# Optimization experiments

Hardware: AMD Instinct MI355X
Metric: run time of the kernel (lower is better)

The kernel has to match this reference:

```python
import jax, jax.numpy as jnp
import numpy as np
import math

T, C = 8192, 1024

def setup_inputs() -> dict:
    key = jax.random.key(0)
    ks = jax.random.split(key, 10)
    s = 1.0 / math.sqrt(C)
    return {
        "x": jax.random.normal(ks[0], (T, C), dtype=jnp.float32),
        "Wq": jax.random.normal(ks[1], (C, C), dtype=jnp.float32) * s,
        "bq": jax.random.normal(ks[2], (C,), dtype=jnp.float32) * s,
        "Wk": jax.random.normal(ks[3], (C, C), dtype=jnp.float32) * s,
        "bk": jax.random.normal(ks[4], (C,), dtype=jnp.float32) * s,
        "Wv": jax.random.normal(ks[5], (C, C), dtype=jnp.float32) * s,
        "bv": jax.random.normal(ks[6], (C,), dtype=jnp.float32) * s,
        "Wp": jax.random.normal(ks[7], (C, C), dtype=jnp.float32) * s,
        "bp": jax.random.normal(ks[8], (C,), dtype=jnp.float32) * s,
    }

def reference(x, Wq, bq, Wk, bk, Wv, bv, Wp, bp):
    # Single-head causal self-attention over an unbatched (T, C) sequence.
    t, c = x.shape
    q = x @ Wq.T + bq          # (T, C)
    k = x @ Wk.T + bk          # (T, C)
    v = x @ Wv.T + bv          # (T, C)
    att = (q @ k.T) / math.sqrt(c)                      # (T, T)
    causal = jnp.tril(jnp.ones((t, t), dtype=bool))
    att = jnp.where(causal, att, -jnp.inf)
    att = jax.nn.softmax(att, axis=-1)
    y = att @ v                                         # (T, C)
    y = y @ Wp.T + bp
    return y
```

## Files before the change

kernel.cpp:

```cpp
#include <hip/hip_runtime.h>
#include <hip/hip_bf16.h>

typedef __bf16 bf16x8 __attribute__((ext_vector_type(8)));
typedef float f32x4 __attribute__((ext_vector_type(4)));

static constexpr int Tn = 8192;
static constexpr int Cn = 1024;

#define DEVI __device__ __forceinline__

DEVI float bf2f(ushort u) { union { uint i; float f; } c; c.i = ((uint)u) << 16; return c.f; }
DEVI ushort f2bf(float f) {
  uint x = __builtin_bit_cast(uint, f);
  x += 0x7fffu + ((x >> 16) & 1u);
  return (ushort)(x >> 16);
}

typedef const __attribute__((address_space(1))) void glb_v;
typedef __attribute__((address_space(3))) void lds_v;

__global__ __launch_bounds__(256) void cast_all(
    const float* __restrict__ x, const float* __restrict__ wq, const float* __restrict__ wk,
    const float* __restrict__ wv, const float* __restrict__ wp,
    ushort* __restrict__ xb, ushort* __restrict__ wqb, ushort* __restrict__ wkb,
    ushort* __restrict__ wvb, ushort* __restrict__ wpb)
{
  const long long NX = (long long)Tn * Cn;
  const long long NW = (long long)Cn * Cn;
  long long i = ((long long)blockIdx.x * 256 + threadIdx.x) * 4;
  const float* src; ushort* dst; long long off;
  if (i < NX) { src = x; dst = xb; off = i; }
  else {
    long long r = i - NX; int seg = (int)(r >> 20); off = r & (NW - 1);
    src = seg == 0 ? wq : seg == 1 ? wk : seg == 2 ? wv : wp;
    dst = seg == 0 ? wqb : seg == 1 ? wkb : seg == 2 ? wvb : wpb;
  }
  float4 v = *reinterpret_cast<const float4*>(src + off);
  ushort4 o; o.x = f2bf(v.x); o.y = f2bf(v.y); o.z = f2bf(v.z); o.w = f2bf(v.w);
  *reinterpret_cast<ushort4*>(dst + off) = o;
}

template<bool OUT_BF16, bool HAS_BIAS, bool CAUSAL_SKIP, bool KLIMIT>
__global__ __launch_bounds__(256, 2)
void gemm_bt(const ushort* __restrict__ A, const ushort* __restrict__ Bt,
             const float* __restrict__ bias, void* __restrict__ outp,
             int M, int N, int K, float scale)
{
  const int bx = blockIdx.x;
  int by = KLIMIT ? (gridDim.y - 1 - blockIdx.y) : blockIdx.y;
  if (CAUSAL_SKIP && by < bx) return;

  __shared__ ushort Als[128 * 64];
  __shared__ ushort Bls[128 * 64];

  const int tid = threadIdx.x;
  const int lane = tid & 63;
  const int wid = tid >> 6;
  const int wr = (wid >> 1) * 64, wc = (wid & 1) * 64;
  const int ln15 = lane & 15, lhi = lane >> 4;
  const int aRow0 = by * 128, bCol0 = bx * 128;

  int Keff = K;
  if (KLIMIT) { int lim = (by + 1) * 128; Keff = lim < K ? lim : K; }
  const int nkt = Keff >> 6;

  f32x4 acc[4][4] = {};

  for (int kt = 0; kt < nkt; ++kt) {
    const int k0 = kt << 6;
#pragma unroll
    for (int i = 0; i < 4; ++i) {
      int c = tid + i * 256;
      int row = c >> 3, kc = c & 7;
      int kcs = kc ^ (row & 7);
      const ushort* ga = A + (size_t)(aRow0 + row) * (size_t)K + (k0 + kcs * 8);
      const ushort* gb = Bt + (size_t)(bCol0 + row) * (size_t)K + (k0 + kcs * 8);
      __builtin_amdgcn_global_load_lds((glb_v*)ga, (lds_v*)(&Als[c * 8]), 16, 0, 0);
      __builtin_amdgcn_global_load_lds((glb_v*)gb, (lds_v*)(&Bls[c * 8]), 16, 0, 0);
    }
    __syncthreads();
#pragma unroll
    for (int kk = 0; kk < 2; ++kk) {
      bf16x8 af[4], bfr[4];
#pragma unroll
      for (int mi = 0; mi < 4; ++mi) {
        int r = wr + mi * 16 + ln15;
        int kc = kk * 4 + lhi;
        int slot = r * 8 + (kc ^ (r & 7));
        af[mi] = *reinterpret_cast<const bf16x8*>(&Als[slot * 8]);
      }
#pragma unroll
      for (int ni = 0; ni < 4; ++ni) {
        int r = wc + ni * 16 + ln15;
        int kc = kk * 4 + lhi;
        int slot = r * 8 + (kc ^ (r & 7));
        bfr[ni] = *reinterpret_cast<const bf16x8*>(&Bls[slot * 8]);
      }
#pragma unroll
      for (int mi = 0; mi < 4; ++mi)
#pragma unroll
        for (int ni = 0; ni < 4; ++ni)
          acc[mi][ni] = __builtin_amdgcn_mfma_f32_16x16x32_bf16(af[mi], bfr[ni], acc[mi][ni], 0, 0, 0);
    }
    __syncthreads();
  }

#pragma unroll
  for (int ni = 0; ni < 4; ++ni) {
    int col = bCol0 + wc + ni * 16 + ln15;
    float bv = HAS_BIAS ? bias[col] : 0.f;
#pragma unroll
    for (int mi = 0; mi < 4; ++mi) {
      f32x4 v = acc[mi][ni];
      int r0 = aRow0 + wr + mi * 16 + lhi * 4;
#pragma unroll
      for (int j = 0; j < 4; ++j) {
        float val = v[j] * scale + bv;
        if (OUT_BF16) ((ushort*)outp)[(size_t)(r0 + j) * N + col] = f2bf(val);
        else          ((float*)outp)[(size_t)(r0 + j) * N + col] = val;
      }
    }
  }
}

__global__ __launch_bounds__(256) void transpose64(const ushort* __restrict__ in,
                                                   ushort* __restrict__ out, int R, int Cin)
{
  __shared__ ushort tile[64][65];
  const int c0 = blockIdx.x * 64, r0 = blockIdx.y * 64;
  const int t = threadIdx.x;
#pragma unroll
  for (int i = t; i < 512; i += 256) {
    int r = i >> 3, kc = i & 7;
    uint4 v = *reinterpret_cast<const uint4*>(in + (size_t)(r0 + r) * Cin + c0 + kc * 8);
    const ushort* u = reinterpret_cast<const ushort*>(&v);
#pragma unroll
    for (int j = 0; j < 8; ++j) tile[r][kc * 8 + j] = u[j];
  }
  __syncthreads();
#pragma unroll
  for (int i = t; i < 512; i += 256) {
    int c = i >> 3, rc = i & 7;
    union { uint4 v; ushort u[8]; } pk;
#pragma unroll
    for (int j = 0; j < 8; ++j) pk.u[j] = tile[rc * 8 + j][c];
    *reinterpret_cast<uint4*>(out + (size_t)(c0 + c) * R + r0 + rc * 8) = pk.v;
  }
}

__global__ __launch_bounds__(256) void softmax_causal(ushort* __restrict__ S, int Td)
{
  const int t = blockIdx.x;
  const int tid = threadIdx.x;
  ushort* row = S + (size_t)t * Td;
  const int L = t + 1;
  const int Lv = L & ~7;

  float sum = 0.f;
  for (int j = tid * 8; j < Lv; j += 2048) {
    uint4 v = *reinterpret_cast<const uint4*>(row + j);
    const ushort* u = reinterpret_cast<const ushort*>(&v);
#pragma unroll
    for (int e = 0; e < 8; ++e) sum += __expf(bf2f(u[e]));
  }
  for (int j = Lv + tid; j < L; j += 256) sum += __expf(bf2f(row[j]));

#pragma unroll
  for (int off = 32; off; off >>= 1) sum += __shfl_down(sum, off);
  __shared__ float red[4];
  if ((tid & 63) == 0) red[tid >> 6] = sum;
  __syncthreads();
  const float inv = 1.f / (red[0] + red[1] + red[2] + red[3]);

  for (int j = tid * 8; j < Lv; j += 2048) {
    uint4 v = *reinterpret_cast<const uint4*>(row + j);
    union { uint4 v; ushort u[8]; } pk;
    const ushort* u = reinterpret_cast<const ushort*>(&v);
#pragma unroll
    for (int e = 0; e < 8; ++e) pk.u[e] = f2bf(__expf(bf2f(u[e])) * inv);
    *reinterpret_cast<uint4*>(row + j) = pk.v;
  }
  for (int j = Lv + tid; j < L; j += 256) row[j] = f2bf(__expf(bf2f(row[j])) * inv);

  const int Za = (L + 7) & ~7;
  for (int j = L + tid; j < Za; j += 256) row[j] = 0;
  uint4 z; z.x = z.y = z.z = z.w = 0u;
  for (int j = Za + tid * 8; j < Td; j += 2048) *reinterpret_cast<uint4*>(row + j) = z;
}

extern "C" void kernel_launch(void* const* d_in, const int* in_sizes, int n_in,
                              void* d_out, int out_size, void* d_ws, size_t ws_size,
                              hipStream_t stream)
{
  (void)in_sizes; (void)n_in; (void)out_size; (void)ws_size;
  const float* x  = (const float*)d_in[0];
  const float* Wq = (const float*)d_in[1];
  const float* bq = (const float*)d_in[2];
  const float* Wk = (const float*)d_in[3];
  const float* bk = (const float*)d_in[4];
  const float* Wv = (const float*)d_in[5];
  const float* bv = (const float*)d_in[6];
  const float* Wp = (const float*)d_in[7];
  const float* bp = (const float*)d_in[8];

  char* w = (char*)d_ws;
  const size_t TC = (size_t)Tn * Cn * 2, CC = (size_t)Cn * Cn * 2;
  ushort* xb  = (ushort*)w; w += TC;
  ushort* wqb = (ushort*)w; w += CC;
  ushort* wkb = (ushort*)w; w += CC;
  ushort* wvb = (ushort*)w; w += CC;
  ushort* wpb = (ushort*)w; w += CC;
  ushort* Qb  = (ushort*)w; w += TC;
  ushort* Kb  = (ushort*)w; w += TC;
  ushort* Vb  = (ushort*)w; w += TC;
  ushort* Vt  = (ushort*)w; w += TC;
  ushort* Yb  = (ushort*)w; w += TC;
  ushort* S   = (ushort*)w; w += (size_t)Tn * Tn * 2;

  cast_all<<<12288, 256, 0, stream>>>(x, Wq, Wk, Wv, Wp, xb, wqb, wkb, wvb, wpb);

  dim3 gp(Cn / 128, Tn / 128);
  gemm_bt<true, true, false, false><<<gp, 256, 0, stream>>>(xb, wqb, bq, Qb, Tn, Cn, Cn, 1.0f);
  gemm_bt<true, true, false, false><<<gp, 256, 0, stream>>>(xb, wkb, bk, Kb, Tn, Cn, Cn, 1.0f);
  gemm_bt<true, true, false, false><<<gp, 256, 0, stream>>>(xb, wvb, bv, Vb, Tn, Cn, Cn, 1.0f);

  transpose64<<<dim3(Cn / 64, Tn / 64), 256, 0, stream>>>(Vb, Vt, Tn, Cn);

  gemm_bt<true, false, true, false><<<dim3(Tn / 128, Tn / 128), 256, 0, stream>>>(
      Qb, Kb, nullptr, S, Tn, Tn, Cn, 0.03125f);

  softmax_causal<<<Tn, 256, 0, stream>>>(S, Tn);

  gemm_bt<true, false, false, true><<<gp, 256, 0, stream>>>(S, Vt, nullptr, Yb, Tn, Cn, Tn, 1.0f);

  gemm_bt<false, true, false, false><<<gp, 256, 0, stream>>>(Yb, wpb, bp, d_out, Tn, Cn, Cn, 1.0f);
}
```

Measured before the change: 370.8 us.

## Replace GEMM with 8-wave double-buffered ping-pong kernel and fuse QKV projection

Replaces the 256-thread single-buffered GEMM with a 512-thread, 8-wave kernel using larger tiles (128x256/256x256), double-buffered LDS, interleaved staged loads, explicit waitcnt/barriers and setprio around MFMA clusters. Q/K/V weights and biases are concatenated so one GEMM produces all three projections. The PV GEMM pairs a long and a short causal row-block per workgroup to balance work. It aims to cut launch count, improve memory/compute overlap and data reuse, at the cost of high register/LDS pressure and complex manual synchronization.

```diff
diff --git a/kernel.cpp b/kernel.cpp
--- a/kernel.cpp
+++ b/kernel.cpp
@@ -19,112 +19,182 @@
 typedef const __attribute__((address_space(1))) void glb_v;
 typedef __attribute__((address_space(3))) void lds_v;
 
+#define BAR()  __builtin_amdgcn_s_barrier()
+#define LGK0() asm volatile("s_waitcnt lgkmcnt(0)" ::: "memory")
+#define VM4()  asm volatile("s_waitcnt vmcnt(4)" ::: "memory")
+#define VM0()  asm volatile("s_waitcnt vmcnt(0)" ::: "memory")
+#define PRIO1() __builtin_amdgcn_s_setprio(1)
+#define PRIO0() __builtin_amdgcn_s_setprio(0)
+
 __global__ __launch_bounds__(256) void cast_all(
     const float* __restrict__ x, const float* __restrict__ wq, const float* __restrict__ wk,
     const float* __restrict__ wv, const float* __restrict__ wp,
-    ushort* __restrict__ xb, ushort* __restrict__ wqb, ushort* __restrict__ wkb,
-    ushort* __restrict__ wvb, ushort* __restrict__ wpb)
+    const float* __restrict__ bq, const float* __restrict__ bk, const float* __restrict__ bv,
+    ushort* __restrict__ xb, ushort* __restrict__ wqkv, ushort* __restrict__ wpb,
+    float* __restrict__ bqkv)
 {
   const long long NX = (long long)Tn * Cn;
   const long long NW = (long long)Cn * Cn;
+  if (blockIdx.x >= 12288) {
+    int id = ((blockIdx.x - 12288) * 256 + threadIdx.x) * 4;
+#pragma unroll
+    for (int e = 0; e < 4; ++e) {
+      int j = id + e;
+      if (j < 3 * Cn) bqkv[j] = j < Cn ? bq[j] : (j < 2 * Cn ? bk[j - Cn] : bv[j - 2 * Cn]);
+    }
+    return;
+  }
   long long i = ((long long)blockIdx.x * 256 + threadIdx.x) * 4;
   const float* src; ushort* dst; long long off;
   if (i < NX) { src = x; dst = xb; off = i; }
   else {
     long long r = i - NX; int seg = (int)(r >> 20); off = r & (NW - 1);
-    src = seg == 0 ? wq : seg == 1 ? wk : seg == 2 ? wv : wp;
-    dst = seg == 0 ? wqb : seg == 1 ? wkb : seg == 2 ? wvb : wpb;
+    if (seg < 3) { src = seg == 0 ? wq : seg == 1 ? wk : wv; dst = wqkv + (size_t)seg * NW; }
+    else         { src = wp; dst = wpb; }
   }
   float4 v = *reinterpret_cast<const float4*>(src + off);
   ushort4 o; o.x = f2bf(v.x); o.y = f2bf(v.y); o.z = f2bf(v.z); o.w = f2bf(v.w);
   *reinterpret_cast<ushort4*>(dst + off) = o;
 }
 
-template<bool OUT_BF16, bool HAS_BIAS, bool CAUSAL_SKIP, bool KLIMIT>
-__global__ __launch_bounds__(256, 2)
-void gemm_bt(const ushort* __restrict__ A, const ushort* __restrict__ Bt,
-             const float* __restrict__ bias, void* __restrict__ outp,
-             int M, int N, int K, float scale)
-{
+template<int BM, int BN, bool OUT_BF16, bool HAS_BIAS, bool CAUSAL_SKIP, bool PVMODE>
+__global__ __launch_bounds__(512, 2)
+void gemm8(const ushort* __restrict__ A, const ushort* __restrict__ Bt,
+           const float* __restrict__ bias, void* __restrict__ outp,
+           int M, int N, int K, int lda, int ldb, int ldc, float scale)
+{
+  constexpr int ASZ = (BM / 2) * 64;
+  constexpr int BSZ = (BN / 2) * 64;
+  constexpr int TOT = 2 * ASZ + 2 * BSZ;
+  constexpr int LA = BM / 128;
+  constexpr int LB = BN / 128;
+  constexpr int MREP = BM / 32;
+  constexpr int NREP = BN / 64;
+  constexpr int MH = MREP / 2;
+
+  __shared__ __align__(16) ushort sm[2 * TOT];
+
+  const int tid = threadIdx.x;
+  const int lane = tid & 63, wid = tid >> 6;
+  const int wm = wid >> 2, wn = wid & 3;
+  const int ln15 = lane & 15, lsec = lane >> 4;
   const int bx = blockIdx.x;
-  int by = KLIMIT ? (gridDim.y - 1 - blockIdx.y) : blockIdx.y;
-  if (CAUSAL_SKIP && by < bx) return;
-
-  __shared__ ushort Als[128 * 64];
-  __shared__ ushort Bls[128 * 64];
-
-  const int tid = threadIdx.x;
-  const int lane = tid & 63;
-  const int wid = tid >> 6;
-  const int wr = (wid >> 1) * 64, wc = (wid & 1) * 64;
-  const int ln15 = lane & 15, lhi = lane >> 4;
-  const int aRow0 = by * 128, bCol0 = bx * 128;
-
-  int Keff = K;
-  if (KLIMIT) { int lim = (by + 1) * 128; Keff = lim < K ? lim : K; }
-  const int nkt = Keff >> 6;
-
-  f32x4 acc[4][4] = {};
-
-  for (int kt = 0; kt < nkt; ++kt) {
-    const int k0 = kt << 6;
-#pragma unroll
-    for (int i = 0; i < 4; ++i) {
-      int c = tid + i * 256;
-      int row = c >> 3, kc = c & 7;
-      int kcs = kc ^ (row & 7);
-      const ushort* ga = A + (size_t)(aRow0 + row) * (size_t)K + (k0 + kcs * 8);
-      const ushort* gb = Bt + (size_t)(bCol0 + row) * (size_t)K + (k0 + kcs * 8);
-      __builtin_amdgcn_global_load_lds((glb_v*)ga, (lds_v*)(&Als[c * 8]), 16, 0, 0);
-      __builtin_amdgcn_global_load_lds((glb_v*)gb, (lds_v*)(&Bls[c * 8]), 16, 0, 0);
+
+  if (CAUSAL_SKIP && (int)blockIdx.y < bx) return;
+
+  const ushort* aB[2] = { &sm[0 * TOT + wm * ASZ], &sm[1 * TOT + wm * ASZ] };
+  const ushort* bB[2] = { &sm[0 * TOT + 2 * ASZ + (wn >> 1) * BSZ],
+                          &sm[1 * TOT + 2 * ASZ + (wn >> 1) * BSZ] };
+
+  const int npairs = PVMODE ? 2 : 1;
+  for (int pr = 0; pr < npairs; ++pr) {
+    const int by = PVMODE ? (pr == 0 ? (int)(2 * gridDim.y - 1 - blockIdx.y)
+                                     : (int)blockIdx.y)
+                          : (int)blockIdx.y;
+    int NT = K >> 6;
+    if (PVMODE) { int kl = (by + 1) * BM; NT = (kl < K ? kl : K) >> 6; }
+    const int rowA0 = by * BM, col0 = bx * BN;
+
+    auto stageA = [&](int b, int h, int t) {
+      const int k0 = (t < NT) ? (t << 6) : 0;
+#pragma unroll
+      for (int i = 0; i < LA; ++i) {
+        int slot = tid + i * 512;
+        int row = slot >> 3, kc = slot & 7;
+        int kcs = kc ^ (row & 7);
+        const ushort* g = A + (size_t)(rowA0 + h * (BM / 2) + row) * (size_t)lda + (k0 + kcs * 8);
+        __builtin_amdgcn_global_load_lds((glb_v*)g, (lds_v*)(&sm[b * TOT + h * ASZ + slot * 8]), 16, 0, 0);
+      }
+    };
+    auto stageB = [&](int b, int h, int t) {
+      const int k0 = (t < NT) ? (t << 6) : 0;
+#pragma unroll
+      for (int i = 0; i < LB; ++i) {
+        int slot = tid + i * 512;
+        int row = slot >> 3, kc = slot & 7;
+        int kcs = kc ^ (row & 7);
+        const ushort* g = Bt + (size_t)(col0 + h * (BN / 2) + row) * (size_t)ldb + (k0 + kcs * 8);
+        __builtin_amdgcn_global_load_lds((glb_v*)g, (lds_v*)(&sm[b * TOT + 2 * ASZ + h * BSZ + slot * 8]), 16, 0, 0);
+      }
+    };
+    auto rdA = [&](const ushort* base, int mi, int ks) -> bf16x8 {
+      int r = mi * 16 + ln15, kc = ks * 4 + lsec;
+      return *reinterpret_cast<const bf16x8*>(base + (r * 8 + (kc ^ (r & 7))) * 8);
+    };
+    auto rdB = [&](const ushort* base, int ni, int ks) -> bf16x8 {
+      int c = (wn & 1) * 64 + ni * 16 + ln15, kc = ks * 4 + lsec;
+      return *reinterpret_cast<const bf16x8*>(base + (c * 8 + (kc ^ (c & 7))) * 8);
+    };
+
+    f32x4 acc[MREP][NREP] = {};
+    bf16x8 a[2 * MH], bl[4], bh[4];
+
+    auto quad = [&](int mb, int nb, bf16x8* bb) {
+#pragma unroll
+      for (int i = 0; i < MH; ++i)
+#pragma unroll
+        for (int j = 0; j < 2; ++j) {
+          acc[mb + i][nb + j] = __builtin_amdgcn_mfma_f32_16x16x32_bf16(a[2 * i], bb[2 * j], acc[mb + i][nb + j], 0, 0, 0);
+          acc[mb + i][nb + j] = __builtin_amdgcn_mfma_f32_16x16x32_bf16(a[2 * i + 1], bb[2 * j + 1], acc[mb + i][nb + j], 0, 0, 0);
+        }
+    };
+#define RD_A_LO(b) { _Pragma("unroll") for (int i = 0; i < MH; ++i) { a[2*i] = rdA(aB[b], i, 0); a[2*i+1] = rdA(aB[b], i, 1); } }
+#define RD_A_HI(b) { _Pragma("unroll") for (int i = 0; i < MH; ++i) { a[2*i] = rdA(aB[b], MH + i, 0); a[2*i+1] = rdA(aB[b], MH + i, 1); } }
+#define RD_B_LO(b) { _Pragma("unroll") for (int i = 0; i < 2; ++i) { bl[2*i] = rdB(bB[b], i, 0); bl[2*i+1] = rdB(bB[b], i, 1); } }
+#define RD_B_HI(b) { _Pragma("unroll") for (int i = 0; i < 2; ++i) { bh[2*i] = rdB(bB[b], 2 + i, 0); bh[2*i+1] = rdB(bB[b], 2 + i, 1); } }
+
+    stageB(0, 0, 0); stageB(0, 1, 0); stageA(0, 0, 0); stageA(0, 1, 0);
+    stageB(1, 0, 1); stageB(1, 1, 1);
+    VM4(); BAR();
+
+    const int NG = NT >> 1;
+    for (int g = 0; g < NG; ++g) {
+      const int t = 2 * g;
+      RD_A_LO(0); RD_B_LO(0); stageA(1, 0, t + 1);
+      BAR(); LGK0(); PRIO1(); quad(0, 0, bl); PRIO0(); BAR();
+      RD_B_HI(0); stageA(1, 1, t + 1);
+      BAR(); LGK0(); PRIO1(); quad(0, 2, bh); PRIO0(); BAR();
+      RD_A_HI(0); stageB(0, 0, t + 2);
+      BAR(); LGK0(); PRIO1(); quad(MH, 2, bh); PRIO0(); BAR();
+      stageB(0, 1, t + 2); VM4();
+      BAR(); LGK0(); PRIO1(); quad(MH, 0, bl); PRIO0(); BAR();
+      RD_A_LO(1); RD_B_LO(1); stageA(0, 0, t + 2);
+      BAR(); LGK0(); PRIO1(); quad(0, 0, bl); PRIO0(); BAR();
+      RD_B_HI(1); stageA(0, 1, t + 2);
+      BAR(); LGK0(); PRIO1(); quad(0, 2, bh); PRIO0(); BAR();
+      RD_A_HI(1); stageB(1, 0, t + 3);
+      BAR(); LGK0(); PRIO1(); quad(MH, 2, bh); PRIO0(); BAR();
+      stageB(1, 1, t + 3); VM4();
+      BAR(); LGK0(); PRIO1(); quad(MH, 0, bl); PRIO0(); BAR();
     }
-    __syncthreads();
-#pragma unroll
-    for (int kk = 0; kk < 2; ++kk) {
-      bf16x8 af[4], bfr[4];
-#pragma unroll
-      for (int mi = 0; mi < 4; ++mi) {
-        int r = wr + mi * 16 + ln15;
-        int kc = kk * 4 + lhi;
-        int slot = r * 8 + (kc ^ (r & 7));
-        af[mi] = *reinterpret_cast<const bf16x8*>(&Als[slot * 8]);
+
+#pragma unroll
+    for (int mi = 0; mi < MREP; ++mi)
+#pragma unroll
+      for (int ni = 0; ni < NREP; ++ni) {
+        int col = col0 + wn * 64 + ni * 16 + ln15;
+        float bv = HAS_BIAS ? bias[col] : 0.f;
+        int r0 = rowA0 + wm * (BM / 2) + mi * 16 + lsec * 4;
+        f32x4 v = acc[mi][ni];
+#pragma unroll
+        for (int j = 0; j < 4; ++j) {
+          float val = v[j] * scale + bv;
+          if (OUT_BF16) ((ushort*)outp)[(size_t)(r0 + j) * (size_t)ldc + col] = f2bf(val);
+          else          ((float*)outp)[(size_t)(r0 + j) * (size_t)ldc + col] = val;
+        }
       }
-#pragma unroll
-      for (int ni = 0; ni < 4; ++ni) {
-        int r = wc + ni * 16 + ln15;
-        int kc = kk * 4 + lhi;
-        int slot = r * 8 + (kc ^ (r & 7));
-        bfr[ni] = *reinterpret_cast<const bf16x8*>(&Bls[slot * 8]);
-      }
-#pragma unroll
-      for (int mi = 0; mi < 4; ++mi)
-#pragma unroll
-        for (int ni = 0; ni < 4; ++ni)
-          acc[mi][ni] = __builtin_amdgcn_mfma_f32_16x16x32_bf16(af[mi], bfr[ni], acc[mi][ni], 0, 0, 0);
-    }
-    __syncthreads();
-  }
-
-#pragma unroll
-  for (int ni = 0; ni < 4; ++ni) {
-    int col = bCol0 + wc + ni * 16 + ln15;
-    float bv = HAS_BIAS ? bias[col] : 0.f;
-#pragma unroll
-    for (int mi = 0; mi < 4; ++mi) {
-      f32x4 v = acc[mi][ni];
-      int r0 = aRow0 + wr + mi * 16 + lhi * 4;
-#pragma unroll
-      for (int j = 0; j < 4; ++j) {
-        float val = v[j] * scale + bv;
-        if (OUT_BF16) ((ushort*)outp)[(size_t)(r0 + j) * N + col] = f2bf(val);
-        else          ((float*)outp)[(size_t)(r0 + j) * N + col] = val;
-      }
-    }
-  }
+    if (PVMODE && pr == 0) { VM0(); BAR(); }
+#undef RD_A_LO
+#undef RD_A_HI
+#undef RD_B_LO
+#undef RD_B_HI
+  }
+  VM0();
 }
 
 __global__ __launch_bounds__(256) void transpose64(const ushort* __restrict__ in,
-                                                   ushort* __restrict__ out, int R, int Cin)
+                                                   ushort* __restrict__ out,
+                                                   int ldin, int ldout)
 {
   __shared__ ushort tile[64][65];
   const int c0 = blockIdx.x * 64, r0 = blockIdx.y * 64;
@@ -132,7 +202,7 @@
 #pragma unroll
   for (int i = t; i < 512; i += 256) {
     int r = i >> 3, kc = i & 7;
-    uint4 v = *reinterpret_cast<const uint4*>(in + (size_t)(r0 + r) * Cin + c0 + kc * 8);
+    uint4 v = *reinterpret_cast<const uint4*>(in + (size_t)(r0 + r) * ldin + c0 + kc * 8);
     const ushort* u = reinterpret_cast<const ushort*>(&v);
 #pragma unroll
     for (int j = 0; j < 8; ++j) tile[r][kc * 8 + j] = u[j];
@@ -144,7 +214,7 @@
     union { uint4 v; ushort u[8]; } pk;
 #pragma unroll
     for (int j = 0; j < 8; ++j) pk.u[j] = tile[rc * 8 + j][c];
-    *reinterpret_cast<uint4*>(out + (size_t)(c0 + c) * R + r0 + rc * 8) = pk.v;
+    *reinterpret_cast<uint4*>(out + (size_t)(c0 + c) * ldout + r0 + rc * 8) = pk.v;
   }
 }
 
@@ -205,33 +275,30 @@
 
   char* w = (char*)d_ws;
   const size_t TC = (size_t)Tn * Cn * 2, CC = (size_t)Cn * Cn * 2;
-  ushort* xb  = (ushort*)w; w += TC;
-  ushort* wqb = (ushort*)w; w += CC;
-  ushort* wkb = (ushort*)w; w += CC;
-  ushort* wvb = (ushort*)w; w += CC;
-  ushort* wpb = (ushort*)w; w += CC;
-  ushort* Qb  = (ushort*)w; w += TC;
-  ushort* Kb  = (ushort*)w; w += TC;
-  ushort* Vb  = (ushort*)w; w += TC;
-  ushort* Vt  = (ushort*)w; w += TC;
-  ushort* Yb  = (ushort*)w; w += TC;
-  ushort* S   = (ushort*)w; w += (size_t)Tn * Tn * 2;
-
-  cast_all<<<12288, 256, 0, stream>>>(x, Wq, Wk, Wv, Wp, xb, wqb, wkb, wvb, wpb);
-
-  dim3 gp(Cn / 128, Tn / 128);
-  gemm_bt<true, true, false, false><<<gp, 256, 0, stream>>>(xb, wqb, bq, Qb, Tn, Cn, Cn, 1.0f);
-  gemm_bt<true, true, false, false><<<gp, 256, 0, stream>>>(xb, wkb, bk, Kb, Tn, Cn, Cn, 1.0f);
-  gemm_bt<true, true, false, false><<<gp, 256, 0, stream>>>(xb, wvb, bv, Vb, Tn, Cn, Cn, 1.0f);
-
-  transpose64<<<dim3(Cn / 64, Tn / 64), 256, 0, stream>>>(Vb, Vt, Tn, Cn);
-
-  gemm_bt<true, false, true, false><<<dim3(Tn / 128, Tn / 128), 256, 0, stream>>>(
-      Qb, Kb, nullptr, S, Tn, Tn, Cn, 0.03125f);
+  ushort* xb   = (ushort*)w; w += TC;
+  ushort* Wqkv = (ushort*)w; w += 3 * CC;
+  ushort* wpb  = (ushort*)w; w += CC;
+  float*  bqkv = (float*)w;  w += 3 * Cn * 4 + 4096;
+  ushort* QKV  = (ushort*)w; w += 3 * TC;
+  ushort* Vt   = (ushort*)w; w += TC;
+  ushort* Yb   = (ushort*)w; w += TC;
+  ushort* S    = (ushort*)w; w += (size_t)Tn * Tn * 2;
+
+  cast_all<<<12291, 256, 0, stream>>>(x, Wq, Wk, Wv, Wp, bq, bk, bv, xb, Wqkv, wpb, bqkv);
+
+  gemm8<128, 256, true, true, false, false><<<dim3(12, 64), 512, 0, stream>>>(
+      xb, Wqkv, bqkv, QKV, Tn, 3 * Cn, Cn, Cn, Cn, 3 * Cn, 1.0f);
+
+  transpose64<<<dim3(Cn / 64, Tn / 64), 256, 0, stream>>>(QKV + 2 * Cn, Vt, 3 * Cn, Tn);
+
+  gemm8<256, 256, true, false, true, false><<<dim3(Tn / 256, Tn / 256), 512, 0, stream>>>(
+      QKV, QKV + Cn, nullptr, S, Tn, Tn, Cn, 3 * Cn, 3 * Cn, Tn, 0.03125f);
 
   softmax_causal<<<Tn, 256, 0, stream>>>(S, Tn);
 
-  gemm_bt<true, false, false, true><<<gp, 256, 0, stream>>>(S, Vt, nullptr, Yb, Tn, Cn, Tn, 1.0f);
-
-  gemm_bt<false, true, false, false><<<gp, 256, 0, stream>>>(Yb, wpb, bp, d_out, Tn, Cn, Cn, 1.0f);
-}
+  gemm8<128, 256, true, false, false, true><<<dim3(Cn / 256, Tn / 256), 512, 0, stream>>>(
+      S, Vt, nullptr, Yb, Tn, Cn, Tn, Tn, Tn, Cn, 1.0f);
+
+  gemm8<128, 256, false, true, false, false><<<dim3(Cn / 256, Tn / 128), 512, 0, stream>>>(
+      Yb, wpb, bp, d_out, Tn, Cn, Cn, Cn, Cn, Cn, 1.0f);
+}
```

Result: slower. 429.0 us (+15.7%).
